# Kernel tuning notes

Measured on AMD Instinct MI355X. Metric: run time of the kernel, lower is better.

## Reference

```python
import jax, jax.numpy as jnp
import numpy as np

LN_EPS = 1e-5


def layer_norm(h, gamma, beta):
    m = jnp.mean(h, axis=-1, keepdims=True)
    v = jnp.mean((h - m) ** 2, axis=-1, keepdims=True)
    return (h - m) * jax.lax.rsqrt(v + LN_EPS) * gamma + beta


def setup_inputs() -> dict:
    key = jax.random.key(0)
    ks = jax.random.split(key, 4)
    B, N, D, H = 4, 256, 256, 256
    x = jax.random.normal(ks[0], (B, N, D), dtype=jnp.float32)
    # Linear(2D, H): weight stored as (in, out) for x @ W
    Wg = jax.random.normal(ks[1], (2 * D, H), dtype=jnp.float32) * (1.0 / np.sqrt(2 * D))
    bg = jnp.zeros((H,), dtype=jnp.float32)
    g_gamma = jnp.ones((H,), dtype=jnp.float32)
    g_beta = jnp.zeros((H,), dtype=jnp.float32)
    Wf = jax.random.normal(ks[2], (H, H), dtype=jnp.float32) * (1.0 / np.sqrt(H))
    bf = jnp.zeros((H,), dtype=jnp.float32)
    f_gamma = jnp.ones((H,), dtype=jnp.float32)
    f_beta = jnp.zeros((H,), dtype=jnp.float32)
    return {"x": x, "Wg": Wg, "bg": bg, "g_gamma": g_gamma, "g_beta": g_beta,
            "Wf": Wf, "bf": bf, "f_gamma": f_gamma, "f_beta": f_beta}


def reference(x, Wg, bg, g_gamma, g_beta, Wf, bf, f_gamma, f_beta):
    B, N, D = x.shape
    # Linear on concat([xi, xj]) == xi @ Wg[:D] + xj @ Wg[D:] ; avoids the (B,N,N,2D) cat.
    a = jnp.einsum('bnd,dh->bnh', x, Wg[:D])   # i-part
    b = jnp.einsum('bnd,dh->bnh', x, Wg[D:])   # j-part
    # pair pre-activation: (B, N_i, N_j, H)
    pre = a[:, :, None, :] + b[:, None, :, :] + bg
    r = layer_norm(jax.nn.relu(pre), g_gamma, g_beta)
    r = jnp.sum(r, axis=(1, 2))                # (B, H)
    rel = layer_norm(jax.nn.relu(r @ Wf + bf), f_gamma, f_beta)  # (B, H)
    return rel[:, None, :] + x                 # broadcast over N
```

## Files before the change

kernel.cpp:

```cpp
#include <hip/hip_runtime.h>

#define LN_EPS 1e-5f

constexpr int Bn = 4, Nn = 256, Dn = 256, Hn = 256;


__global__ __launch_bounds__(512) void gemm_ab_kernel(
    const float* __restrict__ x, const float* __restrict__ Wg,
    const float* __restrict__ bg, float* __restrict__ aA,
    float* __restrict__ bB, float* __restrict__ rC)
{
    int mt = blockIdx.x;
    int half = blockIdx.y;
    int m0 = mt * 4;
    int t = threadIdx.x;

    if (mt == 0 && half == 0) {
        for (int k = t; k < 1024; k += 512) rC[k] = 0.0f;
    }

    __shared__ float xs[4][256];
    __shared__ float accP[8][4][256];

    if (t < 256)
        reinterpret_cast<float4*>(&xs[0][0])[t] =
            reinterpret_cast<const float4*>(x + m0 * Dn)[t];
    __syncthreads();

    int h4 = t & 63;
    int dc = t >> 6;
    const float* Wp = Wg + (half ? Dn * Hn : 0) + h4 * 4;

    float4 acc[4];
#pragma unroll
    for (int m = 0; m < 4; ++m) acc[m] = make_float4(0.f, 0.f, 0.f, 0.f);

#pragma unroll 4
    for (int dd = 0; dd < 32; ++dd) {
        int d = dc * 32 + dd;
        float4 w = *reinterpret_cast<const float4*>(Wp + d * Hn);
#pragma unroll
        for (int m = 0; m < 4; ++m) {
            float xv = xs[m][d];
            acc[m].x = fmaf(xv, w.x, acc[m].x);
            acc[m].y = fmaf(xv, w.y, acc[m].y);
            acc[m].z = fmaf(xv, w.z, acc[m].z);
            acc[m].w = fmaf(xv, w.w, acc[m].w);
        }
    }
#pragma unroll
    for (int m = 0; m < 4; ++m)
        *reinterpret_cast<float4*>(&accP[dc][m][h4 * 4]) = acc[m];
    __syncthreads();

    int h = t & 255;
    int mh = t >> 8;
    float binit = half ? 0.0f : bg[h];
    float* outp = half ? bB : aA;
#pragma unroll
    for (int mi = 0; mi < 2; ++mi) {
        int m = mh * 2 + mi;
        float v = binit;
#pragma unroll
        for (int c = 0; c < 8; ++c) v += accP[c][m][h];
        outp[(m0 + m) * Hn + h] = v;
    }
}

__global__ __launch_bounds__(512, 2) void pair_kernel(
    const float* __restrict__ aA, const float* __restrict__ bB,
    float* __restrict__ rC, float* __restrict__ Cpart)
{
    const int b  = blockIdx.x >> 7;
    const int i0 = (blockIdx.x & 127) * 2;
    const int t  = threadIdx.x;
    const int s  = t >> 4;
    const int p  = t & 15;

    __shared__ float fred[8][16][33];
    __shared__ float wred[8];

    const float* aArow0 = aA + (b * Nn + i0) * Hn + p * 16;
    const float* aArow1 = aArow0 + Hn;
    float4 A0[4], A1[4];
#pragma unroll
    for (int r = 0; r < 4; ++r) {
        A0[r] = *reinterpret_cast<const float4*>(aArow0 + r * 4);
        A1[r] = *reinterpret_cast<const float4*>(aArow1 + r * 4);
    }

    const float* bbase = bB + b * Nn * Hn + p * 16;

    float4 acc0[4], acc1[4];
#pragma unroll
    for (int r = 0; r < 4; ++r) {
        acc0[r] = make_float4(0.f, 0.f, 0.f, 0.f);
        acc1[r] = make_float4(0.f, 0.f, 0.f, 0.f);
    }
    float Csum = 0.f;

    for (int jt = 0; jt < 8; ++jt) {
        const int j = jt * 32 + s;
        const float* rp = bbase + j * Hn;
        float4 bv[4];
#pragma unroll
        for (int r = 0; r < 4; ++r)
            bv[r] = *reinterpret_cast<const float4*>(rp + r * 4);

        float4 v0[4], v1[4];
        float s0 = 0.f, q0 = 0.f, s1 = 0.f, q1 = 0.f;
#pragma unroll
        for (int r = 0; r < 4; ++r) {
            float4 w;
            w.x = fmaxf(A0[r].x + bv[r].x, 0.f);
            w.y = fmaxf(A0[r].y + bv[r].y, 0.f);
            w.z = fmaxf(A0[r].z + bv[r].z, 0.f);
            w.w = fmaxf(A0[r].w + bv[r].w, 0.f);
            v0[r] = w;
            s0 += w.x + w.y + w.z + w.w;
            q0 = fmaf(w.x, w.x, q0); q0 = fmaf(w.y, w.y, q0);
            q0 = fmaf(w.z, w.z, q0); q0 = fmaf(w.w, w.w, q0);
            float4 u;
            u.x = fmaxf(A1[r].x + bv[r].x, 0.f);
            u.y = fmaxf(A1[r].y + bv[r].y, 0.f);
            u.z = fmaxf(A1[r].z + bv[r].z, 0.f);
            u.w = fmaxf(A1[r].w + bv[r].w, 0.f);
            v1[r] = u;
            s1 += u.x + u.y + u.z + u.w;
            q1 = fmaf(u.x, u.x, q1); q1 = fmaf(u.y, u.y, q1);
            q1 = fmaf(u.z, u.z, q1); q1 = fmaf(u.w, u.w, q1);
        }
#pragma unroll
        for (int off = 1; off <= 8; off <<= 1) {
            s0 += __shfl_xor(s0, off, 16);
            q0 += __shfl_xor(q0, off, 16);
            s1 += __shfl_xor(s1, off, 16);
            q1 += __shfl_xor(q1, off, 16);
        }
        float m0 = s0 * (1.f / 256.f), m1 = s1 * (1.f / 256.f);
        float inv0 = rsqrtf(q0 * (1.f / 256.f) - m0 * m0 + LN_EPS);
        float inv1 = rsqrtf(q1 * (1.f / 256.f) - m1 * m1 + LN_EPS);
        if (p == 0) Csum -= m0 * inv0 + m1 * inv1;
#pragma unroll
        for (int r = 0; r < 4; ++r) {
            acc0[r].x = fmaf(inv0, v0[r].x, acc0[r].x);
            acc0[r].y = fmaf(inv0, v0[r].y, acc0[r].y);
            acc0[r].z = fmaf(inv0, v0[r].z, acc0[r].z);
            acc0[r].w = fmaf(inv0, v0[r].w, acc0[r].w);
            acc1[r].x = fmaf(inv1, v1[r].x, acc1[r].x);
            acc1[r].y = fmaf(inv1, v1[r].y, acc1[r].y);
            acc1[r].z = fmaf(inv1, v1[r].z, acc1[r].z);
            acc1[r].w = fmaf(inv1, v1[r].w, acc1[r].w);
        }
    }

#pragma unroll
    for (int r = 0; r < 4; ++r) {
        acc0[r].x += __shfl_xor(acc0[r].x, 16, 64);
        acc0[r].y += __shfl_xor(acc0[r].y, 16, 64);
        acc0[r].z += __shfl_xor(acc0[r].z, 16, 64);
        acc0[r].w += __shfl_xor(acc0[r].w, 16, 64);
        acc1[r].x += __shfl_xor(acc1[r].x, 16, 64);
        acc1[r].y += __shfl_xor(acc1[r].y, 16, 64);
        acc1[r].z += __shfl_xor(acc1[r].z, 16, 64);
        acc1[r].w += __shfl_xor(acc1[r].w, 16, 64);
    }
#pragma unroll
    for (int r = 0; r < 4; ++r) {
        acc0[r].x += __shfl_xor(acc0[r].x, 32, 64);
        acc0[r].y += __shfl_xor(acc0[r].y, 32, 64);
        acc0[r].z += __shfl_xor(acc0[r].z, 32, 64);
        acc0[r].w += __shfl_xor(acc0[r].w, 32, 64);
        acc1[r].x += __shfl_xor(acc1[r].x, 32, 64);
        acc1[r].y += __shfl_xor(acc1[r].y, 32, 64);
        acc1[r].z += __shfl_xor(acc1[r].z, 32, 64);
        acc1[r].w += __shfl_xor(acc1[r].w, 32, 64);
    }
    const int w = t >> 6;
    if ((t & 63) < 16) {
#pragma unroll
        for (int r = 0; r < 4; ++r) {
            fred[w][p][r * 4 + 0] = acc0[r].x;
            fred[w][p][r * 4 + 1] = acc0[r].y;
            fred[w][p][r * 4 + 2] = acc0[r].z;
            fred[w][p][r * 4 + 3] = acc0[r].w;
            fred[w][p][16 + r * 4 + 0] = acc1[r].x;
            fred[w][p][16 + r * 4 + 1] = acc1[r].y;
            fred[w][p][16 + r * 4 + 2] = acc1[r].z;
            fred[w][p][16 + r * 4 + 3] = acc1[r].w;
        }
    }
    float cs = Csum;
#pragma unroll
    for (int off = 32; off >= 1; off >>= 1) cs += __shfl_xor(cs, off, 64);
    if ((t & 63) == 0) wred[w] = cs;
    __syncthreads();

    {
        const int i  = t >> 8;
        const int h  = t & 255;
        const int pp = h >> 4, hh = h & 15;
        float v = 0.f;
#pragma unroll
        for (int ww = 0; ww < 8; ++ww) v += fred[ww][pp][i * 16 + hh];
        atomicAdd(&rC[(b * Nn + 0) * 0 + b * Hn + h + i * 0], 0.0f);
        atomicAdd(&rC[b * Hn + h], v);
    }
    if (t == 0) {
        float cb = 0.f;
#pragma unroll
        for (int ww = 0; ww < 8; ++ww) cb += wred[ww];
        Cpart[blockIdx.x] = cb;
    }
}

__global__ __launch_bounds__(512) void finish_kernel(
    const float* __restrict__ rC, const float* __restrict__ Cpart,
    const float* __restrict__ gg, const float* __restrict__ gb,
    const float* __restrict__ Wf, const float* __restrict__ bfv,
    const float* __restrict__ fg, const float* __restrict__ fb,
    float* __restrict__ rel)
{
    const int b = blockIdx.x;
    const int t = threadIdx.x;
    __shared__ float rs[256];
    __shared__ float ysum[8][260];
    __shared__ float cred[2];
    __shared__ float pS[4], pQ[4];

    float cv = (t < 128) ? Cpart[b * 128 + t] : 0.f;
#pragma unroll
    for (int off = 32; off >= 1; off >>= 1) cv += __shfl_xor(cv, off, 64);
    if (t == 0 || t == 64) cred[t >> 6] = cv;
    __syncthreads();

    if (t < 256) {
        float Cb = cred[0] + cred[1];
        rs[t] = gg[t] * (rC[b * Hn + t] + Cb) + 65536.0f * gb[t];
    }
    __syncthreads();

    const int h4 = t & 63;
    const int kc = t >> 6;
    float4 acc = make_float4(0.f, 0.f, 0.f, 0.f);
    const float* Wp = Wf + h4 * 4;
#pragma unroll 8
    for (int kk = 0; kk < 32; ++kk) {
        int k = kc * 32 + kk;
        float4 w = *reinterpret_cast<const float4*>(Wp + k * Hn);
        float rv = rs[k];
        acc.x = fmaf(rv, w.x, acc.x);
        acc.y = fmaf(rv, w.y, acc.y);
        acc.z = fmaf(rv, w.z, acc.z);
        acc.w = fmaf(rv, w.w, acc.w);
    }
    *reinterpret_cast<float4*>(&ysum[kc][h4 * 4]) = acc;
    __syncthreads();

    float v = 0.f;
    if (t < 256) {
        v = bfv[t];
#pragma unroll
        for (int c = 0; c < 8; ++c) v += ysum[c][t];
        v = fmaxf(v, 0.f);
    }
    float sv = (t < 256) ? v : 0.f;
    float qv = (t < 256) ? v * v : 0.f;
#pragma unroll
    for (int off = 32; off >= 1; off >>= 1) {
        sv += __shfl_xor(sv, off, 64);
        qv += __shfl_xor(qv, off, 64);
    }
    if (t < 256 && (t & 63) == 0) { pS[t >> 6] = sv; pQ[t >> 6] = qv; }
    __syncthreads();

    if (t < 256) {
        float S = pS[0] + pS[1] + pS[2] + pS[3];
        float Q = pQ[0] + pQ[1] + pQ[2] + pQ[3];
        float m = S * (1.f / 256.f);
        float inv = rsqrtf(Q * (1.f / 256.f) - m * m + LN_EPS);
        rel[b * Hn + t] = (v - m) * inv * fg[t] + fb[t];
    }
}

__global__ __launch_bounds__(256) void add_kernel(
    const float* __restrict__ rel, const float* __restrict__ x,
    float* __restrict__ out)
{
    int idx = blockIdx.x * blockDim.x + threadIdx.x;
    int b = idx >> 14;
    int d4 = idx & 63;
    float4 r4 = reinterpret_cast<const float4*>(rel)[b * 64 + d4];
    float4 x4 = reinterpret_cast<const float4*>(x)[idx];
    float4 o;
    o.x = r4.x + x4.x;
    o.y = r4.y + x4.y;
    o.z = r4.z + x4.z;
    o.w = r4.w + x4.w;
    reinterpret_cast<float4*>(out)[idx] = o;
}

extern "C" void kernel_launch(void* const* d_in, const int* in_sizes, int n_in,
                              void* d_out, int out_size, void* d_ws, size_t ws_size,
                              hipStream_t stream)
{
    const float* x   = (const float*)d_in[0];
    const float* Wg  = (const float*)d_in[1];
    const float* bg  = (const float*)d_in[2];
    const float* gg  = (const float*)d_in[3];
    const float* gb  = (const float*)d_in[4];
    const float* Wf  = (const float*)d_in[5];
    const float* bfv = (const float*)d_in[6];
    const float* fg  = (const float*)d_in[7];
    const float* fb  = (const float*)d_in[8];
    float* out = (float*)d_out;

    float* ws    = (float*)d_ws;
    float* aA    = ws;
    float* bB    = ws + 262144;
    float* rC    = ws + 524288;
    float* Cpart = ws + 525312;
    float* rel   = ws + 525824;

    gemm_ab_kernel<<<dim3(256, 2), 512, 0, stream>>>(x, Wg, bg, aA, bB, rC);
    pair_kernel<<<512, 512, 0, stream>>>(aA, bB, rC, Cpart);
    finish_kernel<<<4, 512, 0, stream>>>(rC, Cpart, gg, gb, Wf, bfv, fg, fb, rel);
    add_kernel<<<256, 256, 0, stream>>>(rel, x, out);
}
```

Before: 117.0 us.

## Fuse finish and broadcast-add kernels, halve GEMM row tile, recompute ReLU values

The final LayerNorm/projection kernel now also performs the broadcast add into the output. It runs as 64 blocks that each recompute the per-batch projection and write a 16-row slice, which removes one kernel launch and the rel round trip through global memory. The input GEMM processes 2 rows per block with batched weight loads, doubling the grid. The pair kernel recomputes ReLU outputs instead of holding them in registers to lower register pressure, and drops a redundant zero atomicAdd. The cost is 16x redundant finish computation per batch and more weight reads in the GEMM.

```diff
diff --git a/kernel.cpp b/kernel.cpp
--- a/kernel.cpp
+++ b/kernel.cpp
@@ -12,59 +12,59 @@
 {
     int mt = blockIdx.x;
     int half = blockIdx.y;
-    int m0 = mt * 4;
+    int m0 = mt * 2;
     int t = threadIdx.x;
 
     if (mt == 0 && half == 0) {
         for (int k = t; k < 1024; k += 512) rC[k] = 0.0f;
     }
 
-    __shared__ float xs[4][256];
-    __shared__ float accP[8][4][256];
-
-    if (t < 256)
+    __shared__ float xs[2][256];
+    __shared__ float accP[8][2][256];
+
+    if (t < 128)
         reinterpret_cast<float4*>(&xs[0][0])[t] =
             reinterpret_cast<const float4*>(x + m0 * Dn)[t];
     __syncthreads();
 
-    int h4 = t & 63;
-    int dc = t >> 6;
+    const int h4 = t & 63;
+    const int dc = t >> 6;
     const float* Wp = Wg + (half ? Dn * Hn : 0) + h4 * 4;
 
-    float4 acc[4];
-#pragma unroll
-    for (int m = 0; m < 4; ++m) acc[m] = make_float4(0.f, 0.f, 0.f, 0.f);
-
-#pragma unroll 4
-    for (int dd = 0; dd < 32; ++dd) {
-        int d = dc * 32 + dd;
-        float4 w = *reinterpret_cast<const float4*>(Wp + d * Hn);
-#pragma unroll
-        for (int m = 0; m < 4; ++m) {
-            float xv = xs[m][d];
-            acc[m].x = fmaf(xv, w.x, acc[m].x);
-            acc[m].y = fmaf(xv, w.y, acc[m].y);
-            acc[m].z = fmaf(xv, w.z, acc[m].z);
-            acc[m].w = fmaf(xv, w.w, acc[m].w);
-        }
-    }
-#pragma unroll
-    for (int m = 0; m < 4; ++m)
+    float4 acc[2];
+    acc[0] = make_float4(0.f, 0.f, 0.f, 0.f);
+    acc[1] = make_float4(0.f, 0.f, 0.f, 0.f);
+
+    for (int dd0 = 0; dd0 < 32; dd0 += 8) {
+        float4 w[8];
+#pragma unroll
+        for (int r = 0; r < 8; ++r)
+            w[r] = *reinterpret_cast<const float4*>(Wp + (dc * 32 + dd0 + r) * Hn);
+#pragma unroll
+        for (int r = 0; r < 8; ++r) {
+            int d = dc * 32 + dd0 + r;
+#pragma unroll
+            for (int m = 0; m < 2; ++m) {
+                float xv = xs[m][d];
+                acc[m].x = fmaf(xv, w[r].x, acc[m].x);
+                acc[m].y = fmaf(xv, w[r].y, acc[m].y);
+                acc[m].z = fmaf(xv, w[r].z, acc[m].z);
+                acc[m].w = fmaf(xv, w[r].w, acc[m].w);
+            }
+        }
+    }
+#pragma unroll
+    for (int m = 0; m < 2; ++m)
         *reinterpret_cast<float4*>(&accP[dc][m][h4 * 4]) = acc[m];
     __syncthreads();
 
-    int h = t & 255;
-    int mh = t >> 8;
-    float binit = half ? 0.0f : bg[h];
+    const int h = t & 255;
+    const int m = t >> 8;
+    float v = half ? 0.0f : bg[h];
+#pragma unroll
+    for (int c = 0; c < 8; ++c) v += accP[c][m][h];
     float* outp = half ? bB : aA;
-#pragma unroll
-    for (int mi = 0; mi < 2; ++mi) {
-        int m = mh * 2 + mi;
-        float v = binit;
-#pragma unroll
-        for (int c = 0; c < 8; ++c) v += accP[c][m][h];
-        outp[(m0 + m) * Hn + h] = v;
-    }
+    outp[(m0 + m) * Hn + h] = v;
 }
 
 __global__ __launch_bounds__(512, 2) void pair_kernel(
@@ -107,28 +107,18 @@
         for (int r = 0; r < 4; ++r)
             bv[r] = *reinterpret_cast<const float4*>(rp + r * 4);
 
-        float4 v0[4], v1[4];
         float s0 = 0.f, q0 = 0.f, s1 = 0.f, q1 = 0.f;
 #pragma unroll
         for (int r = 0; r < 4; ++r) {
-            float4 w;
-            w.x = fmaxf(A0[r].x + bv[r].x, 0.f);
-            w.y = fmaxf(A0[r].y + bv[r].y, 0.f);
-            w.z = fmaxf(A0[r].z + bv[r].z, 0.f);
-            w.w = fmaxf(A0[r].w + bv[r].w, 0.f);
-            v0[r] = w;
-            s0 += w.x + w.y + w.z + w.w;
-            q0 = fmaf(w.x, w.x, q0); q0 = fmaf(w.y, w.y, q0);
-            q0 = fmaf(w.z, w.z, q0); q0 = fmaf(w.w, w.w, q0);
-            float4 u;
-            u.x = fmaxf(A1[r].x + bv[r].x, 0.f);
-            u.y = fmaxf(A1[r].y + bv[r].y, 0.f);
-            u.z = fmaxf(A1[r].z + bv[r].z, 0.f);
-            u.w = fmaxf(A1[r].w + bv[r].w, 0.f);
-            v1[r] = u;
-            s1 += u.x + u.y + u.z + u.w;
-            q1 = fmaf(u.x, u.x, q1); q1 = fmaf(u.y, u.y, q1);
-            q1 = fmaf(u.z, u.z, q1); q1 = fmaf(u.w, u.w, q1);
+            float v;
+            v = fmaxf(A0[r].x + bv[r].x, 0.f); s0 += v; q0 = fmaf(v, v, q0);
+            v = fmaxf(A0[r].y + bv[r].y, 0.f); s0 += v; q0 = fmaf(v, v, q0);
+            v = fmaxf(A0[r].z + bv[r].z, 0.f); s0 += v; q0 = fmaf(v, v, q0);
+            v = fmaxf(A0[r].w + bv[r].w, 0.f); s0 += v; q0 = fmaf(v, v, q0);
+            v = fmaxf(A1[r].x + bv[r].x, 0.f); s1 += v; q1 = fmaf(v, v, q1);
+            v = fmaxf(A1[r].y + bv[r].y, 0.f); s1 += v; q1 = fmaf(v, v, q1);
+            v = fmaxf(A1[r].z + bv[r].z, 0.f); s1 += v; q1 = fmaf(v, v, q1);
+            v = fmaxf(A1[r].w + bv[r].w, 0.f); s1 += v; q1 = fmaf(v, v, q1);
         }
 #pragma unroll
         for (int off = 1; off <= 8; off <<= 1) {
@@ -143,14 +133,14 @@
         if (p == 0) Csum -= m0 * inv0 + m1 * inv1;
 #pragma unroll
         for (int r = 0; r < 4; ++r) {
-            acc0[r].x = fmaf(inv0, v0[r].x, acc0[r].x);
-            acc0[r].y = fmaf(inv0, v0[r].y, acc0[r].y);
-            acc0[r].z = fmaf(inv0, v0[r].z, acc0[r].z);
-            acc0[r].w = fmaf(inv0, v0[r].w, acc0[r].w);
-            acc1[r].x = fmaf(inv1, v1[r].x, acc1[r].x);
-            acc1[r].y = fmaf(inv1, v1[r].y, acc1[r].y);
-            acc1[r].z = fmaf(inv1, v1[r].z, acc1[r].z);
-            acc1[r].w = fmaf(inv1, v1[r].w, acc1[r].w);
+            acc0[r].x = fmaf(inv0, fmaxf(A0[r].x + bv[r].x, 0.f), acc0[r].x);
+            acc0[r].y = fmaf(inv0, fmaxf(A0[r].y + bv[r].y, 0.f), acc0[r].y);
+            acc0[r].z = fmaf(inv0, fmaxf(A0[r].z + bv[r].z, 0.f), acc0[r].z);
+            acc0[r].w = fmaf(inv0, fmaxf(A0[r].w + bv[r].w, 0.f), acc0[r].w);
+            acc1[r].x = fmaf(inv1, fmaxf(A1[r].x + bv[r].x, 0.f), acc1[r].x);
+            acc1[r].y = fmaf(inv1, fmaxf(A1[r].y + bv[r].y, 0.f), acc1[r].y);
+            acc1[r].z = fmaf(inv1, fmaxf(A1[r].z + bv[r].z, 0.f), acc1[r].z);
+            acc1[r].w = fmaf(inv1, fmaxf(A1[r].w + bv[r].w, 0.f), acc1[r].w);
         }
     }
 
@@ -203,7 +193,6 @@
         float v = 0.f;
 #pragma unroll
         for (int ww = 0; ww < 8; ++ww) v += fred[ww][pp][i * 16 + hh];
-        atomicAdd(&rC[(b * Nn + 0) * 0 + b * Hn + h + i * 0], 0.0f);
         atomicAdd(&rC[b * Hn + h], v);
     }
     if (t == 0) {
@@ -214,16 +203,18 @@
     }
 }
 
-__global__ __launch_bounds__(512) void finish_kernel(
+__global__ __launch_bounds__(512) void finish_add_kernel(
     const float* __restrict__ rC, const float* __restrict__ Cpart,
     const float* __restrict__ gg, const float* __restrict__ gb,
     const float* __restrict__ Wf, const float* __restrict__ bfv,
     const float* __restrict__ fg, const float* __restrict__ fb,
-    float* __restrict__ rel)
+    const float* __restrict__ x, float* __restrict__ out)
 {
-    const int b = blockIdx.x;
+    const int b = blockIdx.x >> 4;
+    const int slice = blockIdx.x & 15;
     const int t = threadIdx.x;
     __shared__ float rs[256];
+    __shared__ float relS[256];
     __shared__ float ysum[8][260];
     __shared__ float cred[2];
     __shared__ float pS[4], pQ[4];
@@ -279,25 +270,24 @@
         float Q = pQ[0] + pQ[1] + pQ[2] + pQ[3];
         float m = S * (1.f / 256.f);
         float inv = rsqrtf(Q * (1.f / 256.f) - m * m + LN_EPS);
-        rel[b * Hn + t] = (v - m) * inv * fg[t] + fb[t];
-    }
-}
-
-__global__ __launch_bounds__(256) void add_kernel(
-    const float* __restrict__ rel, const float* __restrict__ x,
-    float* __restrict__ out)
-{
-    int idx = blockIdx.x * blockDim.x + threadIdx.x;
-    int b = idx >> 14;
-    int d4 = idx & 63;
-    float4 r4 = reinterpret_cast<const float4*>(rel)[b * 64 + d4];
-    float4 x4 = reinterpret_cast<const float4*>(x)[idx];
-    float4 o;
-    o.x = r4.x + x4.x;
-    o.y = r4.y + x4.y;
-    o.z = r4.z + x4.z;
-    o.w = r4.w + x4.w;
-    reinterpret_cast<float4*>(out)[idx] = o;
+        relS[t] = (v - m) * inv * fg[t] + fb[t];
+    }
+    __syncthreads();
+
+    const int base4 = (b * Nn + slice * 16) * (Hn / 4);
+#pragma unroll
+    for (int kq = 0; kq < 2; ++kq) {
+        int k = kq * 512 + t;
+        int col4 = k & 63;
+        float4 xv = reinterpret_cast<const float4*>(x)[base4 + k];
+        float4 r4 = *reinterpret_cast<const float4*>(&relS[col4 * 4]);
+        float4 o;
+        o.x = xv.x + r4.x;
+        o.y = xv.y + r4.y;
+        o.z = xv.z + r4.z;
+        o.w = xv.w + r4.w;
+        reinterpret_cast<float4*>(out)[base4 + k] = o;
+    }
 }
 
 extern "C" void kernel_launch(void* const* d_in, const int* in_sizes, int n_in,
@@ -320,10 +310,9 @@
     float* bB    = ws + 262144;
     float* rC    = ws + 524288;
     float* Cpart = ws + 525312;
-    float* rel   = ws + 525824;
-
-    gemm_ab_kernel<<<dim3(256, 2), 512, 0, stream>>>(x, Wg, bg, aA, bB, rC);
+
+    gemm_ab_kernel<<<dim3(512, 2), 512, 0, stream>>>(x, Wg, bg, aA, bB, rC);
     pair_kernel<<<512, 512, 0, stream>>>(aA, bB, rC, Cpart);
-    finish_kernel<<<4, 512, 0, stream>>>(rC, Cpart, gg, gb, Wf, bfv, fg, fb, rel);
-    add_kernel<<<256, 256, 0, stream>>>(rel, x, out);
+    finish_add_kernel<<<64, 512, 0, stream>>>(rC, Cpart, gg, gb, Wf, bfv,
+                                              fg, fb, x, out);
 }
```

Result: faster. 112.1 us (-4.2%).
